# Kernel optimization log

Measured on AMD Instinct MI355X. Metric: run time of the kernel, lower is better.

Reference implementation:

```python
import jax, jax.numpy as jnp
import numpy as np

N_NODES = 8192


def _gcn_norm(edge_index, num_nodes):
    # PyG GCNConv default: add self-loops, symmetric normalization.
    src, dst = edge_index[0], edge_index[1]
    loop = jnp.arange(num_nodes, dtype=src.dtype)
    src = jnp.concatenate([src, loop])
    dst = jnp.concatenate([dst, loop])
    deg = jax.ops.segment_sum(jnp.ones_like(dst, dtype=jnp.float32), dst,
                              num_segments=num_nodes)
    dis = jnp.where(deg > 0, jax.lax.rsqrt(jnp.maximum(deg, 1.0)), 0.0)
    norm = dis[src] * dis[dst]  # [E + N]
    return src, dst, norm


def _gcn_conv(x, W, b, src, dst, norm, num_nodes):
    h = x @ W                           # [N, F_out] dense GEMM
    msg = h[src] * norm[:, None]        # gather + scale, [E+N, F_out]
    out = jax.ops.segment_sum(msg, dst, num_segments=num_nodes)  # scatter-add
    return out + b


def setup_inputs() -> dict:
    key = jax.random.key(0)
    ks = jax.random.split(key, 8)
    N, E, F_in, H1, H2, F_out = N_NODES, 65536, 512, 4096, 1024, 10
    x = jax.random.normal(ks[0], (N, F_in), dtype=jnp.float32)
    edge_index = jax.random.randint(ks[1], (2, E), 0, N, dtype=jnp.int64)
    # Glorot-ish scaled weights
    W1 = jax.random.normal(ks[2], (F_in, H1), dtype=jnp.float32) * (1.0 / np.sqrt(F_in))
    b1 = jnp.zeros((H1,), dtype=jnp.float32)
    W2 = jax.random.normal(ks[3], (H1, H2), dtype=jnp.float32) * (1.0 / np.sqrt(H1))
    b2 = jnp.zeros((H2,), dtype=jnp.float32)
    W3 = jax.random.normal(ks[4], (H2, F_out), dtype=jnp.float32) * (1.0 / np.sqrt(H2))
    b3 = jnp.zeros((F_out,), dtype=jnp.float32)
    return {"x": x, "W1": W1, "b1": b1, "W2": W2, "b2": b2,
            "W3": W3, "b3": b3, "edge_index": edge_index}


def reference(x, W1, b1, W2, b2, W3, b3, edge_index):
    N = N_NODES
    src, dst, norm = _gcn_norm(edge_index, N)
    h = _gcn_conv(x.astype(jnp.float32), W1, b1, src, dst, norm, N)
    h = jax.nn.relu(h)  # dropout is identity in eval mode
    h = _gcn_conv(h, W2, b2, src, dst, norm, N)
    h = jax.nn.relu(h)
    h = _gcn_conv(h, W3, b3, src, dst, norm, N)
    return jax.nn.log_softmax(h, axis=1)
```

## Files before the change

### kernel.cpp

```cpp
#include <hip/hip_runtime.h>
#include <math.h>

#define N_NODES 8192
#define N_EDGES 65536
#define F_IN    512
#define HID1    4096
#define HID2    1024
#define F_OUT   10

typedef __bf16 bf16x8 __attribute__((ext_vector_type(8)));
typedef float floatx4 __attribute__((ext_vector_type(4)));

static __device__ __forceinline__ unsigned short f2bf(float f) {
    union { float f; unsigned u; } v; v.f = f;
    unsigned r = v.u + 0x7fffu + ((v.u >> 16) & 1u);
    return (unsigned short)(r >> 16);
}
static __device__ __forceinline__ float bf2f(unsigned short u) {
    union { unsigned u; float f; } v; v.u = ((unsigned)u) << 16;
    return v.f;
}

__global__ void init_kernel(int* __restrict__ deg, int* __restrict__ cnt) {
    int v = blockIdx.x * blockDim.x + threadIdx.x;
    if (v < N_NODES) { deg[v] = 1; cnt[v] = 0; }
}

__global__ void deg_kernel(const int* __restrict__ ei, int* __restrict__ deg) {
    int e = blockIdx.x * blockDim.x + threadIdx.x;
    if (e < N_EDGES) atomicAdd(&deg[ei[N_EDGES + e]], 1);
}

__global__ __launch_bounds__(1024) void scan_kernel(const int* __restrict__ deg,
                                                    int* __restrict__ row_ptr) {
    __shared__ int sums[1024];
    int t = threadIdx.x;
    int base = t * 8;
    int local[8];
    int run = 0;
#pragma unroll
    for (int i = 0; i < 8; i++) { local[i] = run; run += deg[base + i] - 1; }
    sums[t] = run;
    __syncthreads();
    for (int off = 1; off < 1024; off <<= 1) {
        int val = (t >= off) ? sums[t - off] : 0;
        __syncthreads();
        sums[t] += val;
        __syncthreads();
    }
    int offset = (t == 0) ? 0 : sums[t - 1];
#pragma unroll
    for (int i = 0; i < 8; i++) row_ptr[base + i] = offset + local[i];
    if (t == 1023) row_ptr[N_NODES] = sums[1023];
}

__global__ void fill_kernel(const int* __restrict__ ei, const int* __restrict__ deg,
                            const int* __restrict__ row_ptr, int* __restrict__ cnt,
                            int* __restrict__ csr_src, float* __restrict__ csr_w) {
    int e = blockIdx.x * blockDim.x + threadIdx.x;
    if (e < N_EDGES) {
        int s = ei[e];
        int d = ei[N_EDGES + e];
        int slot = row_ptr[d] + atomicAdd(&cnt[d], 1);
        csr_src[slot] = s;
        csr_w[slot] = rsqrtf((float)(deg[s] * deg[d]));
    }
}

__global__ __launch_bounds__(256) void xcvt_kernel(const float* __restrict__ x,
                                                   unsigned short* __restrict__ xb) {
    int i = blockIdx.x * blockDim.x + threadIdx.x;
    float4 a = ((const float4*)x)[i];
    ushort4 o;
    o.x = f2bf(a.x); o.y = f2bf(a.y); o.z = f2bf(a.z); o.w = f2bf(a.w);
    ((ushort4*)xb)[i] = o;
}

__global__ __launch_bounds__(256) void transpose_cvt_kernel(
        const float* __restrict__ W, unsigned short* __restrict__ Wt, int K, int N) {
    __shared__ float t[32][33];
    int tid = threadIdx.x;
    int n0 = blockIdx.x * 32, k0 = blockIdx.y * 32;
    int c = tid & 31, r8 = tid >> 5;
#pragma unroll
    for (int i = 0; i < 4; i++) {
        int r = r8 + i * 8;
        t[r][c] = W[(size_t)(k0 + r) * N + n0 + c];
    }
    __syncthreads();
#pragma unroll
    for (int i = 0; i < 4; i++) {
        int r = r8 + i * 8;
        Wt[(size_t)(n0 + r) * K + k0 + c] = f2bf(t[c][r]);
    }
}

__global__ __launch_bounds__(256) void agg1_kernel(
        const unsigned short* __restrict__ xb, const int* __restrict__ row_ptr,
        const int* __restrict__ csr_src, const float* __restrict__ csr_w,
        const int* __restrict__ deg, unsigned short* __restrict__ out) {
    int v = blockIdx.x * 2 + (threadIdx.x >> 7);
    int t = threadIdx.x & 127;
    const ushort4* x4 = (const ushort4*)xb;
    float sw = 1.0f / (float)deg[v];
    ushort4 a = x4[(size_t)v * 128 + t];
    float ax = sw * bf2f(a.x), ay = sw * bf2f(a.y), az = sw * bf2f(a.z), aw = sw * bf2f(a.w);
    int end = row_ptr[v + 1];
    for (int e = row_ptr[v]; e < end; e++) {
        int s = csr_src[e];
        float w = csr_w[e];
        ushort4 b = x4[(size_t)s * 128 + t];
        ax += w * bf2f(b.x); ay += w * bf2f(b.y); az += w * bf2f(b.z); aw += w * bf2f(b.w);
    }
    ushort4 o;
    o.x = f2bf(ax); o.y = f2bf(ay); o.z = f2bf(az); o.w = f2bf(aw);
    ((ushort4*)out)[(size_t)v * 128 + t] = o;
}

__global__ __launch_bounds__(256) void agg2_kernel(
        const unsigned short* __restrict__ h, const int* __restrict__ row_ptr,
        const int* __restrict__ csr_src, const float* __restrict__ csr_w,
        const int* __restrict__ deg, const float* __restrict__ bias,
        unsigned short* __restrict__ out) {
    int v = blockIdx.x;
    int t = threadIdx.x;
    const ushort4* h4 = (const ushort4*)h;
    float sw = 1.0f / (float)deg[v];
    ushort4 a = h4[(size_t)v * 256 + t];
    float ax = sw * bf2f(a.x), ay = sw * bf2f(a.y), az = sw * bf2f(a.z), aw = sw * bf2f(a.w);
    int end = row_ptr[v + 1];
    for (int e = row_ptr[v]; e < end; e++) {
        int s = csr_src[e];
        float w = csr_w[e];
        ushort4 b = h4[(size_t)s * 256 + t];
        ax += w * bf2f(b.x); ay += w * bf2f(b.y); az += w * bf2f(b.z); aw += w * bf2f(b.w);
    }
    float4 bb = ((const float4*)bias)[t];
    ushort4 o;
    o.x = f2bf(fmaxf(ax + bb.x, 0.0f)); o.y = f2bf(fmaxf(ay + bb.y, 0.0f));
    o.z = f2bf(fmaxf(az + bb.z, 0.0f)); o.w = f2bf(fmaxf(aw + bb.w, 0.0f));
    ((ushort4*)out)[(size_t)v * 256 + t] = o;
}

template <bool OUT_BF16, bool BIAS, bool RELU>
__global__ __launch_bounds__(256) void gemm_mfma_kernel(
        const unsigned short* __restrict__ A,
        const unsigned short* __restrict__ Bt,
        const float* __restrict__ bias,
        void* __restrict__ C,
        int M, int N, int K) {
    __shared__ unsigned short As[128 * 64];
    __shared__ unsigned short Bs[128 * 64];
    int tid = threadIdx.x;
    int wave = tid >> 6, lane = tid & 63;
    int wm = wave >> 1, wn = wave & 1;
    int GN = N >> 7;
    int b = blockIdx.x;
    int ntile = (b >> 3) % GN;
    int mtile = ((b >> 3) / GN) * 8 + (b & 7);
    int m0 = mtile * 128, n0 = ntile * 128;
    int lrow = lane & 15, lquad = lane >> 4;

    floatx4 acc[4][4] = {};

    for (int k0 = 0; k0 < K; k0 += 64) {
#pragma unroll
        for (int j = 0; j < 4; j++) {
            int idx = j * 256 + tid;
            int r = idx >> 3;
            int kc = (idx & 7) ^ (r & 7);
            __builtin_amdgcn_global_load_lds(
                (const __attribute__((address_space(1))) void*)(A + (size_t)(m0 + r) * K + k0 + kc * 8),
                (__attribute__((address_space(3))) void*)(&As[idx * 8]), 16, 0, 0);
            __builtin_amdgcn_global_load_lds(
                (const __attribute__((address_space(1))) void*)(Bt + (size_t)(n0 + r) * K + k0 + kc * 8),
                (__attribute__((address_space(3))) void*)(&Bs[idx * 8]), 16, 0, 0);
        }
        __syncthreads();
#pragma unroll
        for (int kk = 0; kk < 2; kk++) {
            bf16x8 af[4], bfr[4];
#pragma unroll
            for (int mt = 0; mt < 4; mt++) {
                int R = wm * 64 + mt * 16 + lrow;
                int c = kk * 4 + lquad;
                af[mt] = *(const bf16x8*)&As[(R * 8 + (c ^ (R & 7))) * 8];
            }
#pragma unroll
            for (int nt = 0; nt < 4; nt++) {
                int R = wn * 64 + nt * 16 + lrow;
                int c = kk * 4 + lquad;
                bfr[nt] = *(const bf16x8*)&Bs[(R * 8 + (c ^ (R & 7))) * 8];
            }
#pragma unroll
            for (int mt = 0; mt < 4; mt++)
#pragma unroll
                for (int nt = 0; nt < 4; nt++)
                    acc[mt][nt] = __builtin_amdgcn_mfma_f32_16x16x32_bf16(
                        af[mt], bfr[nt], acc[mt][nt], 0, 0, 0);
        }
        __syncthreads();
    }

#pragma unroll
    for (int mt = 0; mt < 4; mt++) {
#pragma unroll
        for (int nt = 0; nt < 4; nt++) {
            int col = n0 + wn * 64 + nt * 16 + lrow;
            float bv = BIAS ? bias[col] : 0.0f;
#pragma unroll
            for (int r = 0; r < 4; r++) {
                int row = m0 + wm * 64 + mt * 16 + lquad * 4 + r;
                float v = acc[mt][nt][r] + bv;
                if (RELU) v = fmaxf(v, 0.0f);
                if (OUT_BF16)
                    ((unsigned short*)C)[(size_t)row * N + col] = f2bf(v);
                else
                    ((float*)C)[(size_t)row * N + col] = v;
            }
        }
    }
}

__global__ __launch_bounds__(256) void gemm3_kernel(const unsigned short* __restrict__ A,
                                                    const float* __restrict__ W,
                                                    float* __restrict__ H3) {
    int r = blockIdx.x;
    int tid = threadIdx.x;
    float acc[F_OUT];
    ushort4 a4 = ((const ushort4*)A)[(size_t)r * 256 + tid];
    float a0 = bf2f(a4.x), a1 = bf2f(a4.y), a2 = bf2f(a4.z), a3 = bf2f(a4.w);
    int k = tid * 4;
#pragma unroll
    for (int c = 0; c < F_OUT; c++)
        acc[c] = a0 * W[k * F_OUT + c] + a1 * W[(k + 1) * F_OUT + c] +
                 a2 * W[(k + 2) * F_OUT + c] + a3 * W[(k + 3) * F_OUT + c];
#pragma unroll
    for (int c = 0; c < F_OUT; c++) {
#pragma unroll
        for (int off = 32; off > 0; off >>= 1) acc[c] += __shfl_down(acc[c], off, 64);
    }
    __shared__ float red[4][F_OUT];
    int wave = tid >> 6, lane = tid & 63;
    if (lane == 0) {
#pragma unroll
        for (int c = 0; c < F_OUT; c++) red[wave][c] = acc[c];
    }
    __syncthreads();
    if (tid < F_OUT) {
        float s = red[0][tid] + red[1][tid] + red[2][tid] + red[3][tid];
        H3[r * F_OUT + tid] = s;
    }
}

__global__ void final_kernel(const float* __restrict__ h3, const int* __restrict__ row_ptr,
                             const int* __restrict__ csr_src, const float* __restrict__ csr_w,
                             const int* __restrict__ deg, const float* __restrict__ b3,
                             float* __restrict__ out) {
    int v = blockIdx.x * blockDim.x + threadIdx.x;
    if (v >= N_NODES) return;
    float sw = 1.0f / (float)deg[v];
    float acc[F_OUT];
#pragma unroll
    for (int c = 0; c < F_OUT; c++) acc[c] = b3[c] + sw * h3[v * F_OUT + c];
    int end = row_ptr[v + 1];
    for (int e = row_ptr[v]; e < end; e++) {
        int s = csr_src[e];
        float w = csr_w[e];
#pragma unroll
        for (int c = 0; c < F_OUT; c++) acc[c] += w * h3[s * F_OUT + c];
    }
    float m = acc[0];
#pragma unroll
    for (int c = 1; c < F_OUT; c++) m = fmaxf(m, acc[c]);
    float ssum = 0.0f;
#pragma unroll
    for (int c = 0; c < F_OUT; c++) ssum += expf(acc[c] - m);
    float l = logf(ssum);
#pragma unroll
    for (int c = 0; c < F_OUT; c++) out[v * F_OUT + c] = acc[c] - m - l;
}

extern "C" void kernel_launch(void* const* d_in, const int* in_sizes, int n_in,
                              void* d_out, int out_size, void* d_ws, size_t ws_size,
                              hipStream_t stream) {
    const float* x  = (const float*)d_in[0];
    const float* W1 = (const float*)d_in[1];
    const float* b1 = (const float*)d_in[2];
    const float* W2 = (const float*)d_in[3];
    const float* b2 = (const float*)d_in[4];
    const float* W3 = (const float*)d_in[5];
    const float* b3 = (const float*)d_in[6];
    const int*   ei = (const int*)d_in[7];
    float* out = (float*)d_out;

    char* p = (char*)d_ws;
    int*   deg     = (int*)p;    p += N_NODES * 4;
    int*   cnt     = (int*)p;    p += N_NODES * 4;
    int*   row_ptr = (int*)p;    p += 33024;
    int*   csr_src = (int*)p;    p += N_EDGES * 4;
    float* csr_w   = (float*)p;  p += N_EDGES * 4;
    float* h3      = (float*)p;  p += N_NODES * F_OUT * 4;
    unsigned short* xb    = (unsigned short*)p; p += (size_t)N_NODES * F_IN * 2;
    unsigned short* agg_x = (unsigned short*)p; p += (size_t)N_NODES * F_IN * 2;
    unsigned short* W1t   = (unsigned short*)p; p += (size_t)HID1 * F_IN * 2;
    unsigned short* W2t   = (unsigned short*)p; p += (size_t)HID2 * HID1 * 2;
    unsigned short* h1    = (unsigned short*)p; p += (size_t)N_NODES * HID1 * 2;
    unsigned short* h2pre = (unsigned short*)p; p += (size_t)N_NODES * HID2 * 2;
    unsigned short* agg2b = (unsigned short*)p; p += (size_t)N_NODES * HID2 * 2;

    init_kernel<<<N_NODES / 256, 256, 0, stream>>>(deg, cnt);
    deg_kernel<<<N_EDGES / 256, 256, 0, stream>>>(ei, deg);
    scan_kernel<<<1, 1024, 0, stream>>>(deg, row_ptr);
    fill_kernel<<<N_EDGES / 256, 256, 0, stream>>>(ei, deg, row_ptr, cnt, csr_src, csr_w);

    xcvt_kernel<<<(N_NODES * F_IN / 4) / 256, 256, 0, stream>>>(x, xb);
    transpose_cvt_kernel<<<dim3(HID1 / 32, F_IN / 32), 256, 0, stream>>>(W1, W1t, F_IN, HID1);
    transpose_cvt_kernel<<<dim3(HID2 / 32, HID1 / 32), 256, 0, stream>>>(W2, W2t, HID1, HID2);

    agg1_kernel<<<N_NODES / 2, 256, 0, stream>>>(xb, row_ptr, csr_src, csr_w, deg, agg_x);
    gemm_mfma_kernel<true, true, true><<<(HID1 / 128) * (N_NODES / 128), 256, 0, stream>>>(
        agg_x, W1t, b1, h1, N_NODES, HID1, F_IN);

    gemm_mfma_kernel<true, false, false><<<(HID2 / 128) * (N_NODES / 128), 256, 0, stream>>>(
        h1, W2t, nullptr, h2pre, N_NODES, HID2, HID1);
    agg2_kernel<<<N_NODES, 256, 0, stream>>>(h2pre, row_ptr, csr_src, csr_w, deg, b2, agg2b);

    gemm3_kernel<<<N_NODES, 256, 0, stream>>>(agg2b, W3, h3);
    final_kernel<<<N_NODES / 256, 256, 0, stream>>>(h3, row_ptr, csr_src, csr_w, deg, b3, out);
}
```

Measured before the change: 318.7 us.

## Fuse prep kernels, replace init with memset, restructure gemm3, unroll aggregation loops

```diff
diff --git a/kernel.cpp b/kernel.cpp
--- a/kernel.cpp
+++ b/kernel.cpp
@@ -7,6 +7,7 @@
 #define HID1    4096
 #define HID2    1024
 #define F_OUT   10
+#define H3_STRIDE 12
 
 typedef __bf16 bf16x8 __attribute__((ext_vector_type(8)));
 typedef float floatx4 __attribute__((ext_vector_type(4)));
@@ -21,25 +22,21 @@
     return v.f;
 }
 
-__global__ void init_kernel(int* __restrict__ deg, int* __restrict__ cnt) {
-    int v = blockIdx.x * blockDim.x + threadIdx.x;
-    if (v < N_NODES) { deg[v] = 1; cnt[v] = 0; }
-}
-
 __global__ void deg_kernel(const int* __restrict__ ei, int* __restrict__ deg) {
     int e = blockIdx.x * blockDim.x + threadIdx.x;
     if (e < N_EDGES) atomicAdd(&deg[ei[N_EDGES + e]], 1);
 }
 
 __global__ __launch_bounds__(1024) void scan_kernel(const int* __restrict__ deg,
-                                                    int* __restrict__ row_ptr) {
+                                                    int* __restrict__ row_ptr,
+                                                    int* __restrict__ cnt) {
     __shared__ int sums[1024];
     int t = threadIdx.x;
     int base = t * 8;
     int local[8];
     int run = 0;
 #pragma unroll
-    for (int i = 0; i < 8; i++) { local[i] = run; run += deg[base + i] - 1; }
+    for (int i = 0; i < 8; i++) { local[i] = run; run += deg[base + i]; cnt[base + i] = 0; }
     sums[t] = run;
     __syncthreads();
     for (int off = 1; off < 1024; off <<= 1) {
@@ -63,24 +60,13 @@
         int d = ei[N_EDGES + e];
         int slot = row_ptr[d] + atomicAdd(&cnt[d], 1);
         csr_src[slot] = s;
-        csr_w[slot] = rsqrtf((float)(deg[s] * deg[d]));
-    }
-}
-
-__global__ __launch_bounds__(256) void xcvt_kernel(const float* __restrict__ x,
-                                                   unsigned short* __restrict__ xb) {
-    int i = blockIdx.x * blockDim.x + threadIdx.x;
-    float4 a = ((const float4*)x)[i];
-    ushort4 o;
-    o.x = f2bf(a.x); o.y = f2bf(a.y); o.z = f2bf(a.z); o.w = f2bf(a.w);
-    ((ushort4*)xb)[i] = o;
-}
-
-__global__ __launch_bounds__(256) void transpose_cvt_kernel(
-        const float* __restrict__ W, unsigned short* __restrict__ Wt, int K, int N) {
-    __shared__ float t[32][33];
-    int tid = threadIdx.x;
-    int n0 = blockIdx.x * 32, k0 = blockIdx.y * 32;
+        csr_w[slot] = rsqrtf((float)((deg[s] + 1) * (deg[d] + 1)));
+    }
+}
+
+static __device__ __forceinline__ void transpose_body(
+        const float* __restrict__ W, unsigned short* __restrict__ Wt,
+        int K, int N, int k0, int n0, int tid, float (*t)[33]) {
     int c = tid & 31, r8 = tid >> 5;
 #pragma unroll
     for (int i = 0; i < 4; i++) {
@@ -92,6 +78,27 @@
     for (int i = 0; i < 4; i++) {
         int r = r8 + i * 8;
         Wt[(size_t)(n0 + r) * K + k0 + c] = f2bf(t[c][r]);
+    }
+}
+
+__global__ __launch_bounds__(256) void prep_kernel(
+        const float* __restrict__ x, unsigned short* __restrict__ xb,
+        const float* __restrict__ W1, unsigned short* __restrict__ W1t,
+        const float* __restrict__ W2, unsigned short* __restrict__ W2t) {
+    __shared__ float t[32][33];
+    int b = blockIdx.x, tid = threadIdx.x;
+    if (b < 4096) {
+        int i = b * 256 + tid;
+        float4 a = ((const float4*)x)[i];
+        ushort4 o;
+        o.x = f2bf(a.x); o.y = f2bf(a.y); o.z = f2bf(a.z); o.w = f2bf(a.w);
+        ((ushort4*)xb)[i] = o;
+    } else if (b < 6144) {
+        int bb = b - 4096;
+        transpose_body(W1, W1t, F_IN, HID1, (bb >> 7) * 32, (bb & 127) * 32, tid, t);
+    } else {
+        int bb = b - 6144;
+        transpose_body(W2, W2t, HID1, HID2, (bb >> 5) * 32, (bb & 31) * 32, tid, t);
     }
 }
 
@@ -102,11 +109,21 @@
     int v = blockIdx.x * 2 + (threadIdx.x >> 7);
     int t = threadIdx.x & 127;
     const ushort4* x4 = (const ushort4*)xb;
-    float sw = 1.0f / (float)deg[v];
+    float sw = 1.0f / (float)(deg[v] + 1);
     ushort4 a = x4[(size_t)v * 128 + t];
     float ax = sw * bf2f(a.x), ay = sw * bf2f(a.y), az = sw * bf2f(a.z), aw = sw * bf2f(a.w);
-    int end = row_ptr[v + 1];
-    for (int e = row_ptr[v]; e < end; e++) {
+    int e = row_ptr[v], end = row_ptr[v + 1];
+    for (; e + 2 <= end; e += 2) {
+        int s0 = csr_src[e], s1 = csr_src[e + 1];
+        float w0 = csr_w[e], w1 = csr_w[e + 1];
+        ushort4 b0 = x4[(size_t)s0 * 128 + t];
+        ushort4 b1 = x4[(size_t)s1 * 128 + t];
+        ax += w0 * bf2f(b0.x) + w1 * bf2f(b1.x);
+        ay += w0 * bf2f(b0.y) + w1 * bf2f(b1.y);
+        az += w0 * bf2f(b0.z) + w1 * bf2f(b1.z);
+        aw += w0 * bf2f(b0.w) + w1 * bf2f(b1.w);
+    }
+    if (e < end) {
         int s = csr_src[e];
         float w = csr_w[e];
         ushort4 b = x4[(size_t)s * 128 + t];
@@ -125,11 +142,21 @@
     int v = blockIdx.x;
     int t = threadIdx.x;
     const ushort4* h4 = (const ushort4*)h;
-    float sw = 1.0f / (float)deg[v];
+    float sw = 1.0f / (float)(deg[v] + 1);
     ushort4 a = h4[(size_t)v * 256 + t];
     float ax = sw * bf2f(a.x), ay = sw * bf2f(a.y), az = sw * bf2f(a.z), aw = sw * bf2f(a.w);
-    int end = row_ptr[v + 1];
-    for (int e = row_ptr[v]; e < end; e++) {
+    int e = row_ptr[v], end = row_ptr[v + 1];
+    for (; e + 2 <= end; e += 2) {
+        int s0 = csr_src[e], s1 = csr_src[e + 1];
+        float w0 = csr_w[e], w1 = csr_w[e + 1];
+        ushort4 b0 = h4[(size_t)s0 * 256 + t];
+        ushort4 b1 = h4[(size_t)s1 * 256 + t];
+        ax += w0 * bf2f(b0.x) + w1 * bf2f(b1.x);
+        ay += w0 * bf2f(b0.y) + w1 * bf2f(b1.y);
+        az += w0 * bf2f(b0.z) + w1 * bf2f(b1.z);
+        aw += w0 * bf2f(b0.w) + w1 * bf2f(b1.w);
+    }
+    if (e < end) {
         int s = csr_src[e];
         float w = csr_w[e];
         ushort4 b = h4[(size_t)s * 256 + t];
@@ -223,33 +250,35 @@
 }
 
 __global__ __launch_bounds__(256) void gemm3_kernel(const unsigned short* __restrict__ A,
-                                                    const float* __restrict__ W,
+                                                    const float* __restrict__ W3,
                                                     float* __restrict__ H3) {
-    int r = blockIdx.x;
+    __shared__ float w3s[HID2 * F_OUT];
     int tid = threadIdx.x;
-    float acc[F_OUT];
-    ushort4 a4 = ((const ushort4*)A)[(size_t)r * 256 + tid];
-    float a0 = bf2f(a4.x), a1 = bf2f(a4.y), a2 = bf2f(a4.z), a3 = bf2f(a4.w);
-    int k = tid * 4;
-#pragma unroll
-    for (int c = 0; c < F_OUT; c++)
-        acc[c] = a0 * W[k * F_OUT + c] + a1 * W[(k + 1) * F_OUT + c] +
-                 a2 * W[(k + 2) * F_OUT + c] + a3 * W[(k + 3) * F_OUT + c];
+    for (int i = tid; i < HID2 * F_OUT; i += 256) w3s[i] = W3[i];
+    __syncthreads();
+    int r = tid >> 3, sub = tid & 7;
+    int row = blockIdx.x * 32 + r;
+    const ushort4* a4p = (const ushort4*)A + (size_t)row * 256;
+    float acc[F_OUT] = {};
+#pragma unroll
+    for (int i = 0; i < 32; i++) {
+        ushort4 a = a4p[i * 8 + sub];
+        int k = i * 32 + sub * 4;
+        float a0 = bf2f(a.x), a1 = bf2f(a.y), a2 = bf2f(a.z), a3 = bf2f(a.w);
+#pragma unroll
+        for (int c = 0; c < F_OUT; c++)
+            acc[c] += a0 * w3s[k * F_OUT + c] + a1 * w3s[(k + 1) * F_OUT + c] +
+                      a2 * w3s[(k + 2) * F_OUT + c] + a3 * w3s[(k + 3) * F_OUT + c];
+    }
 #pragma unroll
     for (int c = 0; c < F_OUT; c++) {
-#pragma unroll
-        for (int off = 32; off > 0; off >>= 1) acc[c] += __shfl_down(acc[c], off, 64);
-    }
-    __shared__ float red[4][F_OUT];
-    int wave = tid >> 6, lane = tid & 63;
-    if (lane == 0) {
-#pragma unroll
-        for (int c = 0; c < F_OUT; c++) red[wave][c] = acc[c];
-    }
-    __syncthreads();
-    if (tid < F_OUT) {
-        float s = red[0][tid] + red[1][tid] + red[2][tid] + red[3][tid];
-        H3[r * F_OUT + tid] = s;
+        acc[c] += __shfl_xor(acc[c], 1, 64);
+        acc[c] += __shfl_xor(acc[c], 2, 64);
+        acc[c] += __shfl_xor(acc[c], 4, 64);
+    }
+    if (sub == 0) {
+#pragma unroll
+        for (int c = 0; c < F_OUT; c++) H3[row * H3_STRIDE + c] = acc[c];
     }
 }
 
@@ -259,16 +288,25 @@
                              float* __restrict__ out) {
     int v = blockIdx.x * blockDim.x + threadIdx.x;
     if (v >= N_NODES) return;
-    float sw = 1.0f / (float)deg[v];
+    const float4* h4 = (const float4*)h3;
+    float sw = 1.0f / (float)(deg[v] + 1);
+    float a[12];
+    *(float4*)&a[0] = h4[v * 3];
+    *(float4*)&a[4] = h4[v * 3 + 1];
+    *(float4*)&a[8] = h4[v * 3 + 2];
     float acc[F_OUT];
 #pragma unroll
-    for (int c = 0; c < F_OUT; c++) acc[c] = b3[c] + sw * h3[v * F_OUT + c];
+    for (int c = 0; c < F_OUT; c++) acc[c] = b3[c] + sw * a[c];
     int end = row_ptr[v + 1];
     for (int e = row_ptr[v]; e < end; e++) {
         int s = csr_src[e];
         float w = csr_w[e];
-#pragma unroll
-        for (int c = 0; c < F_OUT; c++) acc[c] += w * h3[s * F_OUT + c];
+        float bsrc[12];
+        *(float4*)&bsrc[0] = h4[s * 3];
+        *(float4*)&bsrc[4] = h4[s * 3 + 1];
+        *(float4*)&bsrc[8] = h4[s * 3 + 2];
+#pragma unroll
+        for (int c = 0; c < F_OUT; c++) acc[c] += w * bsrc[c];
     }
     float m = acc[0];
 #pragma unroll
@@ -300,7 +338,7 @@
     int*   row_ptr = (int*)p;    p += 33024;
     int*   csr_src = (int*)p;    p += N_EDGES * 4;
     float* csr_w   = (float*)p;  p += N_EDGES * 4;
-    float* h3      = (float*)p;  p += N_NODES * F_OUT * 4;
+    float* h3      = (float*)p;  p += N_NODES * H3_STRIDE * 4;
     unsigned short* xb    = (unsigned short*)p; p += (size_t)N_NODES * F_IN * 2;
     unsigned short* agg_x = (unsigned short*)p; p += (size_t)N_NODES * F_IN * 2;
     unsigned short* W1t   = (unsigned short*)p; p += (size_t)HID1 * F_IN * 2;
@@ -309,14 +347,12 @@
     unsigned short* h2pre = (unsigned short*)p; p += (size_t)N_NODES * HID2 * 2;
     unsigned short* agg2b = (unsigned short*)p; p += (size_t)N_NODES * HID2 * 2;
 
-    init_kernel<<<N_NODES / 256, 256, 0, stream>>>(deg, cnt);
+    hipMemsetAsync(deg, 0, N_NODES * 4, stream);
     deg_kernel<<<N_EDGES / 256, 256, 0, stream>>>(ei, deg);
-    scan_kernel<<<1, 1024, 0, stream>>>(deg, row_ptr);
+    scan_kernel<<<1, 1024, 0, stream>>>(deg, row_ptr, cnt);
     fill_kernel<<<N_EDGES / 256, 256, 0, stream>>>(ei, deg, row_ptr, cnt, csr_src, csr_w);
 
-    xcvt_kernel<<<(N_NODES * F_IN / 4) / 256, 256, 0, stream>>>(x, xb);
-    transpose_cvt_kernel<<<dim3(HID1 / 32, F_IN / 32), 256, 0, stream>>>(W1, W1t, F_IN, HID1);
-    transpose_cvt_kernel<<<dim3(HID2 / 32, HID1 / 32), 256, 0, stream>>>(W2, W2t, HID1, HID2);
+    prep_kernel<<<10240, 256, 0, stream>>>(x, xb, W1, W1t, W2, W2t);
 
     agg1_kernel<<<N_NODES / 2, 256, 0, stream>>>(xb, row_ptr, csr_src, csr_w, deg, agg_x);
     gemm_mfma_kernel<true, true, true><<<(HID1 / 128) * (N_NODES / 128), 256, 0, stream>>>(
@@ -326,6 +362,6 @@
         h1, W2t, nullptr, h2pre, N_NODES, HID2, HID1);
     agg2_kernel<<<N_NODES, 256, 0, stream>>>(h2pre, row_ptr, csr_src, csr_w, deg, b2, agg2b);
 
-    gemm3_kernel<<<N_NODES, 256, 0, stream>>>(agg2b, W3, h3);
+    gemm3_kernel<<<N_NODES / 32, 256, 0, stream>>>(agg2b, W3, h3);
     final_kernel<<<N_NODES / 256, 256, 0, stream>>>(h3, row_ptr, csr_src, csr_w, deg, b3, out);
 }
```

Result: faster. 301.1 us (-5.5%).
